# Kernel tuning notes

Measured on AMD Instinct MI355X. Metric: run time of the kernel, lower is better.

The kernel has to match this reference:

```python
import jax, jax.numpy as jnp
import numpy as np

MODEL_DIM = 512
COND_DIM = 768
HEAD_DIM = 64
N_HEADS = 8


def setup_inputs() -> dict:
    key = jax.random.key(0)
    k1, k2, k3, k4, k5, k6 = jax.random.split(key, 6)
    inner = HEAD_DIM * N_HEADS
    x = jax.random.normal(k1, (16, 4096, MODEL_DIM), dtype=jnp.float32)
    cond = jax.random.normal(k2, (16, 77, COND_DIM), dtype=jnp.float32)
    # nn.Linear weights (out, in); apply as x @ W.T
    s = 0.02
    w_q = jax.random.normal(k3, (inner, MODEL_DIM), dtype=jnp.float32) * s
    w_k = jax.random.normal(k4, (inner, COND_DIM), dtype=jnp.float32) * s
    w_v = jax.random.normal(k5, (inner, COND_DIM), dtype=jnp.float32) * s
    w_o = jax.random.normal(k6, (MODEL_DIM, inner), dtype=jnp.float32) * s
    return {"x": x, "cond": cond, "w_q": w_q, "w_k": w_k, "w_v": w_v, "w_o": w_o}


def reference(x, cond, w_q, w_k, w_v, w_o):
    b, lq, _ = x.shape
    lk = cond.shape[1]
    q = (x @ w_q.T).reshape(b, lq, N_HEADS, HEAD_DIM)
    k = (cond @ w_k.T).reshape(b, lk, N_HEADS, HEAD_DIM)
    v = (cond @ w_v.T).reshape(b, lk, N_HEADS, HEAD_DIM)
    scale = HEAD_DIM ** -0.5
    attn = jnp.einsum('bihd,bjhd->bhij', q, k) * scale  # [b,h,lq,lk]
    attn = jax.nn.softmax(attn, axis=-1)
    out = jnp.einsum('bhij,bjhd->bihd', attn, v).reshape(b, lq, N_HEADS * HEAD_DIM)
    return out @ w_o.T
```

## Files before the change

### kernel.cpp

```cpp
#include <hip/hip_runtime.h>
#include <hip/hip_bf16.h>
#include <stdint.h>


typedef __bf16 bf16_t;
typedef __bf16 bf16x8 __attribute__((ext_vector_type(8)));
typedef float floatx4 __attribute__((ext_vector_type(4)));

#define MFMA16(a, b, c) __builtin_amdgcn_mfma_f32_16x16x32_bf16((a), (b), (c), 0, 0, 0)

__device__ __forceinline__ void gload_lds16(const bf16_t* g, bf16_t* l)
{
    __builtin_amdgcn_global_load_lds(
        (const __attribute__((address_space(1))) void*)g,
        (__attribute__((address_space(3))) void*)l, 16, 0, 0);
}

__global__ __launch_bounds__(256) void cvt_big(
    const float* __restrict__ in, bf16_t* __restrict__ out, long long n8)
{
    for (long long i = (long long)blockIdx.x * 256 + threadIdx.x; i < n8;
         i += (long long)gridDim.x * 256) {
        floatx4 f0 = *(const floatx4*)(in + i * 8);
        floatx4 f1 = *(const floatx4*)(in + i * 8 + 4);
        bf16x8 v;
#pragma unroll
        for (int e = 0; e < 4; e++) { v[e] = (bf16_t)f0[e]; v[e + 4] = (bf16_t)f1[e]; }
        *(bf16x8*)(out + i * 8) = v;
    }
}

struct Cvt5 {
    const float* s[5];
    bf16_t* d[5];
    int n8[5];
};

__global__ __launch_bounds__(256) void cvt_multi(Cvt5 c)
{
    const int seg = blockIdx.y;
    const long long i = (long long)blockIdx.x * 256 + threadIdx.x;
    if (i >= c.n8[seg]) return;
    const float* in = c.s[seg];
    bf16_t* out = c.d[seg];
    floatx4 f0 = *(const floatx4*)(in + i * 8);
    floatx4 f1 = *(const floatx4*)(in + i * 8 + 4);
    bf16x8 v;
#pragma unroll
    for (int e = 0; e < 4; e++) { v[e] = (bf16_t)f0[e]; v[e + 4] = (bf16_t)f1[e]; }
    *(bf16x8*)(out + i * 8) = v;
}

template <bool CF32>
__global__ __launch_bounds__(256) void gemm_bt(
    const bf16_t* __restrict__ A, const bf16_t* __restrict__ B,
    void* __restrict__ Cv, int M, int N, int K)
{
    __shared__ bf16_t As[128 * 32];
    __shared__ bf16_t Bs[128 * 32];

    const int t = threadIdx.x;
    const int l = t & 63;
    const int w = t >> 6;
    const int wm = w >> 1, wn = w & 1;
    const int l15 = l & 15, l4 = l >> 4;
    const int m0 = blockIdx.y * 128, n0 = blockIdx.x * 128;

    floatx4 acc[4][4] = {};

    const bf16_t* ag[2];
    const bf16_t* bg[2];
    bf16_t* al[2];
    bf16_t* bl[2];
#pragma unroll
    for (int i = 0; i < 2; i++) {
        int e = (i * 256 + t) * 8;
        int row = e >> 5, col = e & 31;
        int ra = m0 + row; if (ra > M - 1) ra = M - 1;
        ag[i] = A + (size_t)ra * K + col;
        bg[i] = B + (size_t)(n0 + row) * K + col;
        al[i] = &As[e];
        bl[i] = &Bs[e];
    }

    for (int k0 = 0; k0 < K; k0 += 32) {
#pragma unroll
        for (int i = 0; i < 2; i++) {
            gload_lds16(ag[i] + k0, al[i]);
            gload_lds16(bg[i] + k0, bl[i]);
        }
        __syncthreads();

        bf16x8 af[4], bfr[4];
#pragma unroll
        for (int i = 0; i < 4; i++)
            af[i] = *(const bf16x8*)&As[(wm * 64 + i * 16 + l15) * 32 + l4 * 8];
#pragma unroll
        for (int j = 0; j < 4; j++)
            bfr[j] = *(const bf16x8*)&Bs[(wn * 64 + j * 16 + l15) * 32 + l4 * 8];
#pragma unroll
        for (int i = 0; i < 4; i++)
#pragma unroll
            for (int j = 0; j < 4; j++)
                acc[i][j] = MFMA16(af[i], bfr[j], acc[i][j]);
        __syncthreads();
    }

#pragma unroll
    for (int i = 0; i < 4; i++)
#pragma unroll
        for (int j = 0; j < 4; j++)
#pragma unroll
            for (int r = 0; r < 4; r++) {
                int row = m0 + wm * 64 + i * 16 + l4 * 4 + r;
                int col = n0 + wn * 64 + j * 16 + l15;
                if (row < M) {
                    if (CF32) ((float*)Cv)[(size_t)row * N + col] = acc[i][j][r];
                    else ((bf16_t*)Cv)[(size_t)row * N + col] = (bf16_t)acc[i][j][r];
                }
            }
}

#define LK 77
#define KSTR 72
#define VSTR 104
#define JP 96

__global__ __launch_bounds__(256) void attn_fused(
    bf16_t* QO,
    const bf16_t* __restrict__ Kg,
    const bf16_t* __restrict__ Vg)
{
    __shared__ bf16_t Ks[80 * KSTR];
    __shared__ bf16_t Vs[64 * VSTR];
    __shared__ bf16_t Ps[4 * 32 * VSTR];

    const int t = threadIdx.x;
    const int w = t >> 6, l = t & 63;
    const int l15 = l & 15, l4 = l >> 4;
    const int b = blockIdx.y >> 3, h = blockIdx.y & 7;
    const int q0 = blockIdx.x * 128;

    const bf16_t* qbase =
        QO + ((size_t)(b * 4096 + q0 + w * 32 + l15)) * 512 + h * 64 + l4 * 8;
    bf16x8 aq[2][2];
    aq[0][0] = *(const bf16x8*)qbase;
    aq[0][1] = *(const bf16x8*)(qbase + 32);
    aq[1][0] = *(const bf16x8*)(qbase + 16 * 512);
    aq[1][1] = *(const bf16x8*)(qbase + 16 * 512 + 32);

    for (int idx = t; idx < LK * 8; idx += 256) {
        int j = idx >> 3, c = (idx & 7) * 8;
        *(uint4*)&Ks[j * KSTR + c] =
            *(const uint4*)&Kg[((size_t)(b * LK + j)) * 512 + h * 64 + c];
    }
    for (int idx = t; idx < 3 * KSTR; idx += 256)
        Ks[LK * KSTR + idx] = (bf16_t)0.0f;

    for (int u = t; u < LK * 8; u += 256) {
        int j = u >> 3, d0 = (u & 7) * 8;
        uint4 pk = *(const uint4*)&Vg[((size_t)(b * LK + j)) * 512 + h * 64 + d0];
        const bf16_t* pv = (const bf16_t*)&pk;
#pragma unroll
        for (int e = 0; e < 8; e++)
            Vs[(d0 + e) * VSTR + j] = pv[e];
    }
    for (int idx = t; idx < 64 * (JP - LK); idx += 256) {
        int d = idx / (JP - LK), j = LK + idx % (JP - LK);
        Vs[d * VSTR + j] = (bf16_t)0.0f;
    }
    __syncthreads();

    floatx4 s[2][5];
    __builtin_amdgcn_s_setprio(1);
#pragma unroll
    for (int n = 0; n < 5; n++) {
        bf16x8 b0 = *(const bf16x8*)&Ks[(n * 16 + l15) * KSTR + l4 * 8];
        bf16x8 b1 = *(const bf16x8*)&Ks[(n * 16 + l15) * KSTR + 32 + l4 * 8];
#pragma unroll
        for (int mi = 0; mi < 2; mi++) {
            floatx4 z = {0.f, 0.f, 0.f, 0.f};
            z = MFMA16(aq[mi][0], b0, z);
            z = MFMA16(aq[mi][1], b1, z);
            s[mi][n] = z;
        }
    }
    __builtin_amdgcn_s_setprio(0);

    const float scale = 0.125f;
    float p[2][5][4], linv[2][4];
#pragma unroll
    for (int mi = 0; mi < 2; mi++)
#pragma unroll
        for (int r = 0; r < 4; r++) {
            float smax = -1e30f;
#pragma unroll
            for (int n = 0; n < 5; n++) {
                float v = s[mi][n][r] * scale;
                if (n == 4 && (64 + l15) >= LK) v = -1e30f;
                p[mi][n][r] = v;
                smax = fmaxf(smax, v);
            }
#pragma unroll
            for (int off = 1; off < 16; off <<= 1)
                smax = fmaxf(smax, __shfl_xor(smax, off, 64));
            float sum = 0.f;
#pragma unroll
            for (int n = 0; n < 5; n++) {
                float e2 = __expf(p[mi][n][r] - smax);
                p[mi][n][r] = e2;
                sum += e2;
            }
#pragma unroll
            for (int off = 1; off < 16; off <<= 1)
                sum += __shfl_xor(sum, off, 64);
            linv[mi][r] = 1.0f / sum;
        }

    bf16_t* pw = Ps + w * 32 * VSTR;
#pragma unroll
    for (int mi = 0; mi < 2; mi++)
#pragma unroll
        for (int r = 0; r < 4; r++) {
            int row = mi * 16 + l4 * 4 + r;
#pragma unroll
            for (int n = 0; n < 5; n++)
                pw[row * VSTR + n * 16 + l15] = (bf16_t)(p[mi][n][r] * linv[mi][r]);
            pw[row * VSTR + 80 + l15] = (bf16_t)0.0f;
        }
    __syncthreads();

    bf16x8 ap[2][3];
#pragma unroll
    for (int mi = 0; mi < 2; mi++)
#pragma unroll
        for (int ks = 0; ks < 3; ks++)
            ap[mi][ks] = *(const bf16x8*)&pw[(mi * 16 + l15) * VSTR + ks * 32 + l4 * 8];
#pragma unroll
    for (int n2 = 0; n2 < 4; n2++) {
        bf16x8 bv[3];
#pragma unroll
        for (int ks = 0; ks < 3; ks++)
            bv[ks] = *(const bf16x8*)&Vs[(n2 * 16 + l15) * VSTR + ks * 32 + l4 * 8];
        floatx4 o[2];
        __builtin_amdgcn_s_setprio(1);
#pragma unroll
        for (int mi = 0; mi < 2; mi++) {
            floatx4 z = {0.f, 0.f, 0.f, 0.f};
#pragma unroll
            for (int ks = 0; ks < 3; ks++)
                z = MFMA16(ap[mi][ks], bv[ks], z);
            o[mi] = z;
        }
        __builtin_amdgcn_s_setprio(0);
#pragma unroll
        for (int mi = 0; mi < 2; mi++)
#pragma unroll
            for (int r = 0; r < 4; r++) {
                int q = q0 + w * 32 + mi * 16 + l4 * 4 + r;
                QO[((size_t)(b * 4096 + q)) * 512 + h * 64 + n2 * 16 + l15] =
                    (bf16_t)o[mi][r];
            }
    }
}

extern "C" void kernel_launch(void* const* d_in, const int* in_sizes, int n_in,
                              void* d_out, int out_size, void* d_ws, size_t ws_size,
                              hipStream_t stream)
{
    const float* x    = (const float*)d_in[0];
    const float* cond = (const float*)d_in[1];
    const float* w_q  = (const float*)d_in[2];
    const float* w_k  = (const float*)d_in[3];
    const float* w_v  = (const float*)d_in[4];
    const float* w_o  = (const float*)d_in[5];
    float* out = (float*)d_out;

    const int Mq  = 16 * 4096;
    const int Mkv = 16 * 77;

    bf16_t* Qb  = (bf16_t*)d_ws;
    bf16_t* Kb  = Qb + (size_t)Mq * 512;
    bf16_t* Vb  = Kb + (size_t)Mkv * 512;
    bf16_t* Wob = Vb + (size_t)Mkv * 512;

    bf16_t* Xb  = (bf16_t*)d_out;
    bf16_t* Cb  = Xb  + (size_t)Mq * 512;
    bf16_t* Wqb = Cb  + (size_t)Mkv * 768;
    bf16_t* Wkb = Wqb + (size_t)512 * 512;
    bf16_t* Wvb = Wkb + (size_t)512 * 768;

    const long long n8x = (long long)Mq * 512 / 8;
    cvt_big<<<dim3(2048), 256, 0, stream>>>(x, Xb, n8x);

    Cvt5 c;
    c.s[0] = cond; c.d[0] = Cb;  c.n8[0] = Mkv * 768 / 8;
    c.s[1] = w_q;  c.d[1] = Wqb; c.n8[1] = 512 * 512 / 8;
    c.s[2] = w_k;  c.d[2] = Wkb; c.n8[2] = 512 * 768 / 8;
    c.s[3] = w_v;  c.d[3] = Wvb; c.n8[3] = 512 * 768 / 8;
    c.s[4] = w_o;  c.d[4] = Wob; c.n8[4] = 512 * 512 / 8;
    cvt_multi<<<dim3((118272 + 255) / 256, 5), 256, 0, stream>>>(c);

    gemm_bt<false><<<dim3(4, Mq / 128), 256, 0, stream>>>(Xb, Wqb, Qb, Mq, 512, 512);
    gemm_bt<false><<<dim3(4, (Mkv + 127) / 128), 256, 0, stream>>>(Cb, Wkb, Kb, Mkv, 512, 768);
    gemm_bt<false><<<dim3(4, (Mkv + 127) / 128), 256, 0, stream>>>(Cb, Wvb, Vb, Mkv, 512, 768);

    attn_fused<<<dim3(32, 128), 256, 0, stream>>>(Qb, Kb, Vb);

    gemm_bt<true><<<dim3(4, Mq / 128), 256, 0, stream>>>(Qb, Wob, out, Mq, 512, 512);
}
```

Before: 445.2 us.

## Merge conversion kernels, fuse K/V projections, deepen GEMM K-tile, remap workgroups

The two fp32-to-bf16 conversion launches become one kernel with two grid rows, and the K and V projections become a single GEMM over a concatenated weight that writes an interleaved KV buffer read by attention. The GEMM now loads a 64-wide K slice per barrier (two 32-wide sub-tiles in LDS) and remaps workgroup ids in groups of 8, which is meant to improve locality across compute units. Together these cut launch count and barrier overhead, at the cost of twice the LDS per GEMM block, which may lower occupancy.

```diff
diff --git a/kernel.cpp b/kernel.cpp
--- a/kernel.cpp
+++ b/kernel.cpp
@@ -16,39 +16,39 @@
         (__attribute__((address_space(3))) void*)l, 16, 0, 0);
 }
 
-__global__ __launch_bounds__(256) void cvt_big(
-    const float* __restrict__ in, bf16_t* __restrict__ out, long long n8)
-{
-    for (long long i = (long long)blockIdx.x * 256 + threadIdx.x; i < n8;
-         i += (long long)gridDim.x * 256) {
-        floatx4 f0 = *(const floatx4*)(in + i * 8);
-        floatx4 f1 = *(const floatx4*)(in + i * 8 + 4);
-        bf16x8 v;
-#pragma unroll
-        for (int e = 0; e < 4; e++) { v[e] = (bf16_t)f0[e]; v[e + 4] = (bf16_t)f1[e]; }
-        *(bf16x8*)(out + i * 8) = v;
-    }
-}
-
-struct Cvt5 {
+struct CvtArgs {
     const float* s[5];
     bf16_t* d[5];
-    int n8[5];
 };
 
-__global__ __launch_bounds__(256) void cvt_multi(Cvt5 c)
-{
-    const int seg = blockIdx.y;
-    const long long i = (long long)blockIdx.x * 256 + threadIdx.x;
-    if (i >= c.n8[seg]) return;
-    const float* in = c.s[seg];
-    bf16_t* out = c.d[seg];
+__device__ __forceinline__ void cvt8(const float* in, bf16_t* out, long long i)
+{
     floatx4 f0 = *(const floatx4*)(in + i * 8);
     floatx4 f1 = *(const floatx4*)(in + i * 8 + 4);
     bf16x8 v;
 #pragma unroll
     for (int e = 0; e < 4; e++) { v[e] = (bf16_t)f0[e]; v[e + 4] = (bf16_t)f1[e]; }
     *(bf16x8*)(out + i * 8) = v;
+}
+
+__global__ __launch_bounds__(256) void cvt_all(
+    const float* __restrict__ x, bf16_t* __restrict__ xb, long long n8x, CvtArgs c)
+{
+    if (blockIdx.y == 0) {
+        for (long long i = (long long)blockIdx.x * 256 + threadIdx.x; i < n8x;
+             i += (long long)2048 * 256)
+            cvt8(x, xb, i);
+    } else {
+        int gid = blockIdx.x, seg, base;
+        if      (gid <  462) { seg = 0; base = 0;   }
+        else if (gid <  590) { seg = 1; base = 462; }
+        else if (gid <  782) { seg = 2; base = 590; }
+        else if (gid <  974) { seg = 3; base = 782; }
+        else if (gid < 1102) { seg = 4; base = 974; }
+        else return;
+        long long i = (long long)(gid - base) * 256 + threadIdx.x;
+        cvt8(c.s[seg], c.d[seg], i);
+    }
 }
 
 template <bool CF32>
@@ -56,26 +56,36 @@
     const bf16_t* __restrict__ A, const bf16_t* __restrict__ B,
     void* __restrict__ Cv, int M, int N, int K)
 {
-    __shared__ bf16_t As[128 * 32];
-    __shared__ bf16_t Bs[128 * 32];
+    __shared__ bf16_t As[2 * 128 * 32];
+    __shared__ bf16_t Bs[2 * 128 * 32];
 
     const int t = threadIdx.x;
     const int l = t & 63;
     const int w = t >> 6;
     const int wm = w >> 1, wn = w & 1;
     const int l15 = l & 15, l4 = l >> 4;
-    const int m0 = blockIdx.y * 128, n0 = blockIdx.x * 128;
+
+    const int nbx = gridDim.x;
+    const int nwg = nbx * gridDim.y;
+    int lid = blockIdx.y * nbx + blockIdx.x;
+    if ((nwg & 7) == 0) {
+        const int cpx = nwg >> 3;
+        lid = (lid & 7) * cpx + (lid >> 3);
+    }
+    const int m0 = (lid / nbx) * 128, n0 = (lid % nbx) * 128;
 
     floatx4 acc[4][4] = {};
 
-    const bf16_t* ag[2];
-    const bf16_t* bg[2];
-    bf16_t* al[2];
-    bf16_t* bl[2];
-#pragma unroll
-    for (int i = 0; i < 2; i++) {
+    const bf16_t* ag[4];
+    const bf16_t* bg[4];
+    bf16_t* al[4];
+    bf16_t* bl[4];
+#pragma unroll
+    for (int i = 0; i < 4; i++) {
         int e = (i * 256 + t) * 8;
-        int row = e >> 5, col = e & 31;
+        int kk = e >> 12;
+        int row = (e & 4095) >> 5;
+        int col = kk * 32 + (e & 31);
         int ra = m0 + row; if (ra > M - 1) ra = M - 1;
         ag[i] = A + (size_t)ra * K + col;
         bg[i] = B + (size_t)(n0 + row) * K + col;
@@ -83,26 +93,29 @@
         bl[i] = &Bs[e];
     }
 
-    for (int k0 = 0; k0 < K; k0 += 32) {
-#pragma unroll
-        for (int i = 0; i < 2; i++) {
+    for (int k0 = 0; k0 < K; k0 += 64) {
+#pragma unroll
+        for (int i = 0; i < 4; i++) {
             gload_lds16(ag[i] + k0, al[i]);
             gload_lds16(bg[i] + k0, bl[i]);
         }
         __syncthreads();
 
-        bf16x8 af[4], bfr[4];
-#pragma unroll
-        for (int i = 0; i < 4; i++)
-            af[i] = *(const bf16x8*)&As[(wm * 64 + i * 16 + l15) * 32 + l4 * 8];
-#pragma unroll
-        for (int j = 0; j < 4; j++)
-            bfr[j] = *(const bf16x8*)&Bs[(wn * 64 + j * 16 + l15) * 32 + l4 * 8];
-#pragma unroll
-        for (int i = 0; i < 4; i++)
+#pragma unroll
+        for (int kk = 0; kk < 2; kk++) {
+            bf16x8 af[4], bfr[4];
+#pragma unroll
+            for (int i = 0; i < 4; i++)
+                af[i] = *(const bf16x8*)&As[kk * 4096 + (wm * 64 + i * 16 + l15) * 32 + l4 * 8];
 #pragma unroll
             for (int j = 0; j < 4; j++)
-                acc[i][j] = MFMA16(af[i], bfr[j], acc[i][j]);
+                bfr[j] = *(const bf16x8*)&Bs[kk * 4096 + (wn * 64 + j * 16 + l15) * 32 + l4 * 8];
+#pragma unroll
+            for (int i = 0; i < 4; i++)
+#pragma unroll
+                for (int j = 0; j < 4; j++)
+                    acc[i][j] = MFMA16(af[i], bfr[j], acc[i][j]);
+        }
         __syncthreads();
     }
 
@@ -122,14 +135,14 @@
 }
 
 #define LK 77
+#define KVSTR 1024
 #define KSTR 72
 #define VSTR 104
 #define JP 96
 
 __global__ __launch_bounds__(256) void attn_fused(
     bf16_t* QO,
-    const bf16_t* __restrict__ Kg,
-    const bf16_t* __restrict__ Vg)
+    const bf16_t* __restrict__ KVg)
 {
     __shared__ bf16_t Ks[80 * KSTR];
     __shared__ bf16_t Vs[64 * VSTR];
@@ -149,17 +162,20 @@
     aq[1][0] = *(const bf16x8*)(qbase + 16 * 512);
     aq[1][1] = *(const bf16x8*)(qbase + 16 * 512 + 32);
 
+    const bf16_t* Kg = KVg;
+    const bf16_t* Vg = KVg + 512;
+
     for (int idx = t; idx < LK * 8; idx += 256) {
         int j = idx >> 3, c = (idx & 7) * 8;
         *(uint4*)&Ks[j * KSTR + c] =
-            *(const uint4*)&Kg[((size_t)(b * LK + j)) * 512 + h * 64 + c];
+            *(const uint4*)&Kg[((size_t)(b * LK + j)) * KVSTR + h * 64 + c];
     }
     for (int idx = t; idx < 3 * KSTR; idx += 256)
         Ks[LK * KSTR + idx] = (bf16_t)0.0f;
 
     for (int u = t; u < LK * 8; u += 256) {
         int j = u >> 3, d0 = (u & 7) * 8;
-        uint4 pk = *(const uint4*)&Vg[((size_t)(b * LK + j)) * 512 + h * 64 + d0];
+        uint4 pk = *(const uint4*)&Vg[((size_t)(b * LK + j)) * KVSTR + h * 64 + d0];
         const bf16_t* pv = (const bf16_t*)&pk;
 #pragma unroll
         for (int e = 0; e < 8; e++)
@@ -280,32 +296,26 @@
     const int Mkv = 16 * 77;
 
     bf16_t* Qb  = (bf16_t*)d_ws;
-    bf16_t* Kb  = Qb + (size_t)Mq * 512;
-    bf16_t* Vb  = Kb + (size_t)Mkv * 512;
-    bf16_t* Wob = Vb + (size_t)Mkv * 512;
-
-    bf16_t* Xb  = (bf16_t*)d_out;
-    bf16_t* Cb  = Xb  + (size_t)Mq * 512;
-    bf16_t* Wqb = Cb  + (size_t)Mkv * 768;
-    bf16_t* Wkb = Wqb + (size_t)512 * 512;
-    bf16_t* Wvb = Wkb + (size_t)512 * 768;
-
-    const long long n8x = (long long)Mq * 512 / 8;
-    cvt_big<<<dim3(2048), 256, 0, stream>>>(x, Xb, n8x);
-
-    Cvt5 c;
-    c.s[0] = cond; c.d[0] = Cb;  c.n8[0] = Mkv * 768 / 8;
-    c.s[1] = w_q;  c.d[1] = Wqb; c.n8[1] = 512 * 512 / 8;
-    c.s[2] = w_k;  c.d[2] = Wkb; c.n8[2] = 512 * 768 / 8;
-    c.s[3] = w_v;  c.d[3] = Wvb; c.n8[3] = 512 * 768 / 8;
-    c.s[4] = w_o;  c.d[4] = Wob; c.n8[4] = 512 * 512 / 8;
-    cvt_multi<<<dim3((118272 + 255) / 256, 5), 256, 0, stream>>>(c);
+    bf16_t* KVb = Qb + (size_t)Mq * 512;
+    bf16_t* Wob = KVb + (size_t)Mkv * 1024;
+
+    bf16_t* Xb   = (bf16_t*)d_out;
+    bf16_t* Cb   = Xb  + (size_t)Mq * 512;
+    bf16_t* Wqb  = Cb  + (size_t)Mkv * 768;
+    bf16_t* Wkvb = Wqb + (size_t)512 * 512;
+
+    CvtArgs c;
+    c.s[0] = cond; c.d[0] = Cb;
+    c.s[1] = w_q;  c.d[1] = Wqb;
+    c.s[2] = w_k;  c.d[2] = Wkvb;
+    c.s[3] = w_v;  c.d[3] = Wkvb + (size_t)512 * 768;
+    c.s[4] = w_o;  c.d[4] = Wob;
+    cvt_all<<<dim3(2048, 2), 256, 0, stream>>>(x, Xb, (long long)Mq * 512 / 8, c);
 
     gemm_bt<false><<<dim3(4, Mq / 128), 256, 0, stream>>>(Xb, Wqb, Qb, Mq, 512, 512);
-    gemm_bt<false><<<dim3(4, (Mkv + 127) / 128), 256, 0, stream>>>(Cb, Wkb, Kb, Mkv, 512, 768);
-    gemm_bt<false><<<dim3(4, (Mkv + 127) / 128), 256, 0, stream>>>(Cb, Wvb, Vb, Mkv, 512, 768);
-
-    attn_fused<<<dim3(32, 128), 256, 0, stream>>>(Qb, Kb, Vb);
+    gemm_bt<false><<<dim3(8, (Mkv + 127) / 128), 256, 0, stream>>>(Cb, Wkvb, KVb, Mkv, 1024, 768);
+
+    attn_fused<<<dim3(32, 128), 256, 0, stream>>>(Qb, KVb);
 
     gemm_bt<true><<<dim3(4, Mq / 128), 256, 0, stream>>>(Qb, Wob, out, Mq, 512, 512);
 }
```

Measured after the change: 403.3 us. 1.1x faster.
